# Kernel tuning notes

Hardware: AMD Instinct MI355X
Metric: run time of the kernel (lower is better)

Reference implementation:

```python
import jax, jax.numpy as jnp
import numpy as np

B, W, C_BLK, N_EMBD, N_HEADS = 512, 128, 24, 32, 2


def setup_inputs() -> dict:
    key = jax.random.key(0)
    k1, k2, k3, k4 = jax.random.split(key, 4)
    x = jax.random.normal(k1, (B, W, C_BLK, N_EMBD), dtype=jnp.float32)
    x_end_idx = jax.random.randint(k2, (B, W), 0, C_BLK, dtype=jnp.int32)
    # nn.Linear(n_embd, 3*n_embd, bias=False): store transposed so y = x @ w
    w_attn = jax.random.normal(k3, (N_EMBD, 3 * N_EMBD), dtype=jnp.float32) * (1.0 / np.sqrt(N_EMBD))
    w_proj = jax.random.normal(k4, (N_EMBD, N_EMBD), dtype=jnp.float32) * (1.0 / np.sqrt(N_EMBD))
    return {"x": x, "x_end_idx": x_end_idx, "w_attn": w_attn, "w_proj": w_proj}


def reference(x, x_end_idx, w_attn, w_proj):
    # x: [B, W, c, C]; causal self-attention over the char axis c, per (batch, word).
    Bd, Wd, c, C = x.shape
    H = N_HEADS
    D = C // H
    qkv = x @ w_attn                               # [B, W, c, 3C]
    q, k, v = jnp.split(qkv, 3, axis=-1)
    # [B, W, H, c, D]
    q = q.reshape(Bd, Wd, c, H, D).transpose(0, 1, 3, 2, 4)
    k = k.reshape(Bd, Wd, c, H, D).transpose(0, 1, 3, 2, 4)
    v = v.reshape(Bd, Wd, c, H, D).transpose(0, 1, 3, 2, 4)
    scale = 1.0 / jnp.sqrt(jnp.asarray(D, dtype=x.dtype))
    scores = jnp.einsum('bwhqd,bwhkd->bwhqk', q, k) * scale   # [B, W, H, c, c]
    causal = jnp.tril(jnp.ones((c, c), dtype=bool))
    scores = jnp.where(causal, scores, jnp.asarray(-jnp.inf, dtype=scores.dtype))
    att = jax.nn.softmax(scores, axis=-1)
    out = jnp.einsum('bwhqk,bwhkd->bwhqd', att, v)            # [B, W, H, c, D]
    out = out.transpose(0, 1, 3, 2, 4).reshape(Bd, Wd, c, C)
    out = out @ w_proj                                        # c_proj (dropout in eval mode = identity)
    out = x + out                                             # residual
    # Vectorized last-token gather: pick out[b, w, x_end_idx[b, w], :]
    idx = x_end_idx[:, :, None, None].astype(jnp.int32)       # [B, W, 1, 1]
    samples = jnp.take_along_axis(out, jnp.broadcast_to(idx, (Bd, Wd, 1, C)), axis=2)
    return samples.squeeze(2)                                 # [B, W, C]
```

## Files before the change

kernel.cpp:

```cpp
#include <hip/hip_runtime.h>


#define CB      24
#define CC      32
#define DD      16
#define THREEC  96
#define NBW     (512 * 128)
#define WPB     4
#define XSS     34
#define NREP    2

__device__ __align__(16) float4 g_M4[2][8][CC];
__device__ __align__(16) float4 g_P4[2][8][CC];

__global__ void precompute_mp(const float* __restrict__ w_attn,
                              const float* __restrict__ w_proj)
{
    const int idx = blockIdx.x * 256 + threadIdx.x;
    const int h = idx >> 8, e4 = (idx >> 5) & 7, c = idx & 31;
    float m[4], p[4];
    #pragma unroll
    for (int k = 0; k < 4; ++k) {
        const int e = 4 * e4 + k;
        float mm = 0.f, pp = 0.f;
        #pragma unroll
        for (int d = 0; d < DD; ++d) {
            const int i = DD * h + d;
            mm = fmaf(w_attn[e * THREEC + i],          w_attn[c * THREEC + CC + i], mm);
            pp = fmaf(w_attn[e * THREEC + 2 * CC + i], w_proj[i * CC + c],          pp);
        }
        m[k] = 0.25f * mm;
        p[k] = pp;
    }
    g_M4[h][e4][c] = make_float4(m[0], m[1], m[2], m[3]);
    g_P4[h][e4][c] = make_float4(p[0], p[1], p[2], p[3]);
}

struct __align__(16) WaveSmem {
    float xs[CB][XSS];
    float rks[2][CC];
    float ps[2][CC];
    float ys[2][CC];
};

__device__ __forceinline__ void wave_fence() {
    __asm__ volatile("s_waitcnt lgkmcnt(0)" ::: "memory");
}

__global__ __launch_bounds__(256, 8) void char_attn_kernel(
    const float* __restrict__ x,
    const int*   __restrict__ xend,
    float*       __restrict__ out)
{
    __shared__ WaveSmem sm[WPB];

    const int tid  = threadIdx.x;
    const int lane = tid & 63;
    const int wave = tid >> 6;
    WaveSmem& S = sm[wave];

    const int i32  = lane & 31;
    const int half = lane >> 5;

    const int sbid = __builtin_amdgcn_readfirstlane(blockIdx.x * WPB + wave);
    const int sq   = __builtin_amdgcn_readfirstlane(xend[sbid]);
    const int L    = sq + 1;

    const float* __restrict__ xb = x + (size_t)sbid * (CB * CC);
    const float* __restrict__ xq = xb + sq * CC;

    float4 xqv[8];
    #pragma unroll
    for (int e = 0; e < 8; ++e) xqv[e] = *(const float4*)(xq + 4 * e);

    {
        const float2* xb2 = (const float2*)xb;
        const int n2 = L * (CC / 2);
        #pragma unroll
        for (int i = 0; i < 6; ++i) {
            const int t = lane + 64 * i;
            float2 v = make_float2(0.f, 0.f);
            if (t < n2) v = xb2[t];
            const int r = t >> 4, c = (t & 15) * 2;
            *(float2*)&S.xs[r][c] = v;
        }
    }
    wave_fence();

    #pragma unroll 1
    for (int rep = 0; rep < NREP; ++rep) {

        {
            float a0 = 0.f, a1 = 0.f, a2 = 0.f, a3 = 0.f;
            #pragma unroll
            for (int e4 = 0; e4 < 8; ++e4) {
                const float4 mv = g_M4[half][e4][i32];
                a0 = fmaf(mv.x, xqv[e4].x, a0);
                a1 = fmaf(mv.y, xqv[e4].y, a1);
                a2 = fmaf(mv.z, xqv[e4].z, a2);
                a3 = fmaf(mv.w, xqv[e4].w, a3);
            }
            S.rks[half][i32] = (a0 + a1) + (a2 + a3);
        }
        wave_fence();

        float rsum;
        {
            float e = 0.f;
            {
                const float4* rk4 = (const float4*)&S.rks[half][0];
                float a0 = 0.f, a1 = 0.f, a2 = 0.f, a3 = 0.f;
                #pragma unroll
                for (int e4 = 0; e4 < 8; ++e4) {
                    const float4 rv = rk4[e4];
                    const float2 x0 = *(const float2*)&S.xs[i32][e4 * 4];
                    const float2 x1 = *(const float2*)&S.xs[i32][e4 * 4 + 2];
                    a0 = fmaf(rv.x, x0.x, a0);
                    a1 = fmaf(rv.y, x0.y, a1);
                    a2 = fmaf(rv.z, x1.x, a2);
                    a3 = fmaf(rv.w, x1.y, a3);
                }
                e = (i32 <= sq) ? __expf((a0 + a1) + (a2 + a3)) : 0.f;
            }
            S.ps[half][i32] = e;
            float sum = e;
            #pragma unroll
            for (int off = 16; off >= 1; off >>= 1)
                sum += __shfl_xor(sum, off);
            rsum = __fdividef(1.f, sum);
        }
        wave_fence();

        {
            float4 pr[6];
            const float4* ps4 = (const float4*)&S.ps[half][0];
            #pragma unroll
            for (int i = 0; i < 6; ++i) pr[i] = ps4[i];
            const float* pf = (const float*)&pr[0];
            float a0 = 0.f, a1 = 0.f;
            #pragma unroll
            for (int j = 0; j < CB; j += 2) {
                a0 = fmaf(pf[j],     S.xs[j][i32],     a0);
                a1 = fmaf(pf[j + 1], S.xs[j + 1][i32], a1);
            }
            S.ys[half][i32] = (a0 + a1) * rsum;
        }
        wave_fence();

        {
            const float4* y4 = (const float4*)&S.ys[half][0];
            float a0 = 0.f, a1 = 0.f, a2 = 0.f, a3 = 0.f;
            #pragma unroll
            for (int e4 = 0; e4 < 8; ++e4) {
                const float4 pv = g_P4[half][e4][i32];
                const float4 yv = y4[e4];
                a0 = fmaf(pv.x, yv.x, a0);
                a1 = fmaf(pv.y, yv.y, a1);
                a2 = fmaf(pv.z, yv.z, a2);
                a3 = fmaf(pv.w, yv.w, a3);
            }
            float t = (a0 + a1) + (a2 + a3);
            t += __shfl_xor(t, 32);
            if (lane < CC)
                out[(size_t)sbid * CC + i32] = t + S.xs[sq][i32];
        }
    }
}

extern "C" void kernel_launch(void* const* d_in, const int* in_sizes, int n_in,
                              void* d_out, int out_size, void* d_ws, size_t ws_size,
                              hipStream_t stream) {
    const float* x      = (const float*)d_in[0];
    const int*   xend   = (const int*)d_in[1];
    const float* w_attn = (const float*)d_in[2];
    const float* w_proj = (const float*)d_in[3];
    float* out = (float*)d_out;

    precompute_mp<<<dim3(2), dim3(256), 0, stream>>>(w_attn, w_proj);
    char_attn_kernel<<<dim3(NBW / WPB), dim3(WPB * 64), 0, stream>>>(
        x, xend, out);
}
```

Measured before the change: 325.5 us.

## Process four word slots per wave with register prefetch of next slot

```diff
diff --git a/kernel.cpp b/kernel.cpp
--- a/kernel.cpp
+++ b/kernel.cpp
@@ -7,8 +7,9 @@
 #define THREEC  96
 #define NBW     (512 * 128)
 #define WPB     4
+#define NPW     4
+#define NBLK    (NBW / (WPB * NPW))
 #define XSS     34
-#define NREP    2
 
 __device__ __align__(16) float4 g_M4[2][8][CC];
 __device__ __align__(16) float4 g_P4[2][8][CC];
@@ -62,33 +63,57 @@
     const int i32  = lane & 31;
     const int half = lane >> 5;
 
-    const int sbid = __builtin_amdgcn_readfirstlane(blockIdx.x * WPB + wave);
-    const int sq   = __builtin_amdgcn_readfirstlane(xend[sbid]);
-    const int L    = sq + 1;
-
-    const float* __restrict__ xb = x + (size_t)sbid * (CB * CC);
-    const float* __restrict__ xq = xb + sq * CC;
-
+    const int sbase = __builtin_amdgcn_readfirstlane(
+                          (blockIdx.x * WPB + wave) * NPW);
+    const int* __restrict__ xe = xend + sbase;
+
+    int sq  = __builtin_amdgcn_readfirstlane(xe[0]);
+    int sqn = __builtin_amdgcn_readfirstlane(xe[1]);
+
+    float4 pf[3];
+    {
+        const float4* xp = (const float4*)(x + (size_t)sbase * (CB * CC));
+        const int n4 = (sq + 1) * 8;
+        #pragma unroll
+        for (int i = 0; i < 3; ++i) {
+            const int t = lane + 64 * i;
+            pf[i] = make_float4(0.f, 0.f, 0.f, 0.f);
+            if (t < n4) pf[i] = xp[t];
+        }
+    }
     float4 xqv[8];
-    #pragma unroll
-    for (int e = 0; e < 8; ++e) xqv[e] = *(const float4*)(xq + 4 * e);
-
     {
-        const float2* xb2 = (const float2*)xb;
-        const int n2 = L * (CC / 2);
-        #pragma unroll
-        for (int i = 0; i < 6; ++i) {
+        const float* xq0 = x + (size_t)sbase * (CB * CC) + sq * CC;
+        #pragma unroll
+        for (int e = 0; e < 8; ++e) xqv[e] = *(const float4*)(xq0 + 4 * e);
+    }
+
+    #pragma unroll 1
+    for (int k = 0; k < NPW; ++k) {
+        const int pid = sbase + k;
+        const float* __restrict__ xb = x + (size_t)pid * (CB * CC);
+        const int n4 = (sq + 1) * 8;
+
+        #pragma unroll
+        for (int i = 0; i < 3; ++i) {
             const int t = lane + 64 * i;
-            float2 v = make_float2(0.f, 0.f);
-            if (t < n2) v = xb2[t];
-            const int r = t >> 4, c = (t & 15) * 2;
-            *(float2*)&S.xs[r][c] = v;
-        }
-    }
-    wave_fence();
-
-    #pragma unroll 1
-    for (int rep = 0; rep < NREP; ++rep) {
+            const float4 v = (t < n4) ? pf[i] : make_float4(0.f, 0.f, 0.f, 0.f);
+            const int r = t >> 3, c = (t & 7) * 4;
+            *(float2*)&S.xs[r][c]     = make_float2(v.x, v.y);
+            *(float2*)&S.xs[r][c + 2] = make_float2(v.z, v.w);
+        }
+
+        if (k + 1 < NPW) {
+            const float4* xp = (const float4*)(xb + CB * CC);
+            const int n4n = (sqn + 1) * 8;
+            #pragma unroll
+            for (int i = 0; i < 3; ++i) {
+                const int t = lane + 64 * i;
+                if (t < n4n) pf[i] = xp[t];
+            }
+        }
+        const int sqf = __builtin_amdgcn_readfirstlane(
+                            xe[(k + 2 < NPW) ? k + 2 : NPW - 1]);
 
         {
             float a0 = 0.f, a1 = 0.f, a2 = 0.f, a3 = 0.f;
@@ -104,24 +129,28 @@
         }
         wave_fence();
 
+        float4 xqn[8];
+        if (k + 1 < NPW) {
+            const float* xqp = xb + CB * CC + sqn * CC;
+            #pragma unroll
+            for (int e = 0; e < 8; ++e) xqn[e] = *(const float4*)(xqp + 4 * e);
+        }
+
         float rsum;
         {
-            float e = 0.f;
-            {
-                const float4* rk4 = (const float4*)&S.rks[half][0];
-                float a0 = 0.f, a1 = 0.f, a2 = 0.f, a3 = 0.f;
-                #pragma unroll
-                for (int e4 = 0; e4 < 8; ++e4) {
-                    const float4 rv = rk4[e4];
-                    const float2 x0 = *(const float2*)&S.xs[i32][e4 * 4];
-                    const float2 x1 = *(const float2*)&S.xs[i32][e4 * 4 + 2];
-                    a0 = fmaf(rv.x, x0.x, a0);
-                    a1 = fmaf(rv.y, x0.y, a1);
-                    a2 = fmaf(rv.z, x1.x, a2);
-                    a3 = fmaf(rv.w, x1.y, a3);
-                }
-                e = (i32 <= sq) ? __expf((a0 + a1) + (a2 + a3)) : 0.f;
-            }
+            const float4* rk4 = (const float4*)&S.rks[half][0];
+            float a0 = 0.f, a1 = 0.f, a2 = 0.f, a3 = 0.f;
+            #pragma unroll
+            for (int e4 = 0; e4 < 8; ++e4) {
+                const float4 rv = rk4[e4];
+                const float2 x0 = *(const float2*)&S.xs[i32][e4 * 4];
+                const float2 x1 = *(const float2*)&S.xs[i32][e4 * 4 + 2];
+                a0 = fmaf(rv.x, x0.x, a0);
+                a1 = fmaf(rv.y, x0.y, a1);
+                a2 = fmaf(rv.z, x1.x, a2);
+                a3 = fmaf(rv.w, x1.y, a3);
+            }
+            const float e = (i32 <= sq) ? __expf((a0 + a1) + (a2 + a3)) : 0.f;
             S.ps[half][i32] = e;
             float sum = e;
             #pragma unroll
@@ -136,12 +165,12 @@
             const float4* ps4 = (const float4*)&S.ps[half][0];
             #pragma unroll
             for (int i = 0; i < 6; ++i) pr[i] = ps4[i];
-            const float* pf = (const float*)&pr[0];
+            const float* pfv = (const float*)&pr[0];
             float a0 = 0.f, a1 = 0.f;
             #pragma unroll
             for (int j = 0; j < CB; j += 2) {
-                a0 = fmaf(pf[j],     S.xs[j][i32],     a0);
-                a1 = fmaf(pf[j + 1], S.xs[j + 1][i32], a1);
+                a0 = fmaf(pfv[j],     S.xs[j][i32],     a0);
+                a1 = fmaf(pfv[j + 1], S.xs[j + 1][i32], a1);
             }
             S.ys[half][i32] = (a0 + a1) * rsum;
         }
@@ -161,8 +190,15 @@
             }
             float t = (a0 + a1) + (a2 + a3);
             t += __shfl_xor(t, 32);
+            const float resid = xb[sq * CC + i32];
             if (lane < CC)
-                out[(size_t)sbid * CC + i32] = t + S.xs[sq][i32];
+                out[(size_t)pid * CC + i32] = t + resid;
+        }
+
+        sq = sqn; sqn = sqf;
+        if (k + 1 < NPW) {
+            #pragma unroll
+            for (int e = 0; e < 8; ++e) xqv[e] = xqn[e];
         }
     }
 }
@@ -177,6 +213,6 @@
     float* out = (float*)d_out;
 
     precompute_mp<<<dim3(2), dim3(256), 0, stream>>>(w_attn, w_proj);
-    char_attn_kernel<<<dim3(NBW / WPB), dim3(WPB * 64), 0, stream>>>(
+    char_attn_kernel<<<dim3(NBLK), dim3(WPB * 64), 0, stream>>>(
         x, xend, out);
 }
```

Result: faster. 303.2 us (-6.8%).
